# Kernel tuning notes

Hardware: AMD Instinct MI355X
Metric: run time of the kernel (lower is better)

Reference implementation:

```python
import jax, jax.numpy as jnp
import numpy as np
from jax import lax

WIN_SIZE = 11
WIN_SIGMA = 1.5
DATA_RANGE = 1.0
K1, K2 = 0.01, 0.03


def _gauss_1d(win_size, sigma):
    coords = jnp.arange(win_size, dtype=jnp.float32) - win_size // 2
    g = jnp.exp(-(coords ** 2) / (2.0 * sigma ** 2))
    return g / jnp.sum(g)


def _gauss_filter(x, win):
    # Separable depthwise gaussian blur, VALID padding (matches pytorch_msssim).
    C = x.shape[1]
    kh = jnp.tile(win.reshape(1, 1, -1, 1), (C, 1, 1, 1))  # (C,1,k,1)
    kw = jnp.tile(win.reshape(1, 1, 1, -1), (C, 1, 1, 1))  # (C,1,1,k)
    dn = ('NCHW', 'OIHW', 'NCHW')
    x = lax.conv_general_dilated(x, kh, (1, 1), 'VALID',
                                 dimension_numbers=dn, feature_group_count=C)
    x = lax.conv_general_dilated(x, kw, (1, 1), 'VALID',
                                 dimension_numbers=dn, feature_group_count=C)
    return x


def _ssim(X, Y, win, data_range):
    C1 = (K1 * data_range) ** 2
    C2 = (K2 * data_range) ** 2
    mu1 = _gauss_filter(X, win)
    mu2 = _gauss_filter(Y, win)
    mu1_sq = mu1 * mu1
    mu2_sq = mu2 * mu2
    mu1_mu2 = mu1 * mu2
    sigma1_sq = _gauss_filter(X * X, win) - mu1_sq
    sigma2_sq = _gauss_filter(Y * Y, win) - mu2_sq
    sigma12 = _gauss_filter(X * Y, win) - mu1_mu2
    cs_map = (2.0 * sigma12 + C2) / (sigma1_sq + sigma2_sq + C2)
    ssim_map = ((2.0 * mu1_mu2 + C1) / (mu1_sq + mu2_sq + C1)) * cs_map
    return jnp.mean(ssim_map)


def setup_inputs() -> dict:
    key = jax.random.key(0)
    k1, k2 = jax.random.split(key)
    shape = (16, 3, 384, 512)
    pred = jax.random.uniform(k1, shape, dtype=jnp.float32)
    target = jax.random.uniform(k2, shape, dtype=jnp.float32)
    return {"pred": pred, "target": target}


def reference(pred, target):
    win = _gauss_1d(WIN_SIZE, WIN_SIGMA)
    ssim_val = _ssim(pred, target, win, DATA_RANGE)
    return 1.0 - ssim_val
```

## Files before the change

### kernel.cpp

```cpp
#include <hip/hip_runtime.h>
#include <math.h>

#define WIN 11
#define IMG_H 384
#define IMG_W 512
#define OUT_H (IMG_H - WIN + 1)
#define OUT_W (IMG_W - WIN + 1)
#define RPW 2
#define NPAIRS 187
#define NIMG 48
#define TOTAL_PAIRS (NPAIRS * NIMG)
#define WPB 4
#define NBLOCKS 2248
#define BPX 281
#define NBUCKETS 256

typedef float v2 __attribute__((ext_vector_type(2)));

struct GaussW { float g[WIN]; };

__device__ __forceinline__ v2 shfl_v2(v2 v, int src) {
    v2 r; r.x = __shfl(v.x, src, 64); r.y = __shfl(v.y, src, 64); return r;
}

__device__ __forceinline__ void horiz11_v2(const v2 (&A)[8], v2 (&out)[8],
                                           int lane, const GaussW& gw)
{
    v2 V[18];
    #pragma unroll
    for (int j = 0; j < 8; ++j) V[j] = A[j];
    #pragma unroll
    for (int j = 0; j < 8; ++j) V[8 + j] = shfl_v2(A[j], lane + 1);
    V[16] = shfl_v2(A[0], lane + 2);
    V[17] = shfl_v2(A[1], lane + 2);
    #pragma unroll
    for (int j = 0; j < 8; ++j) {
        v2 o = 0.f;
        #pragma unroll
        for (int k = 0; k < WIN; ++k) {
            v2 g = gw.g[k];
            o = __builtin_elementwise_fma(g, V[j + k], o);
        }
        out[j] = o;
    }
}

__device__ __forceinline__ void horiz11_f(const float (&A)[8], float (&out)[8],
                                          int lane, const GaussW& gw)
{
    float V[18];
    #pragma unroll
    for (int j = 0; j < 8; ++j) V[j] = A[j];
    #pragma unroll
    for (int j = 0; j < 8; ++j) V[8 + j] = __shfl(A[j], lane + 1, 64);
    V[16] = __shfl(A[0], lane + 2, 64);
    V[17] = __shfl(A[1], lane + 2, 64);
    #pragma unroll
    for (int j = 0; j < 8; ++j) {
        float o = 0.f;
        #pragma unroll
        for (int k = 0; k < WIN; ++k) o = fmaf(gw.g[k], V[j + k], o);
        out[j] = o;
    }
}

__global__ __launch_bounds__(256) void ssim_fused_kernel(
    const float* __restrict__ X, const float* __restrict__ Y,
    double* __restrict__ accum, GaussW gw)
{
    const int wave = threadIdx.x >> 6;
    const int lane = threadIdx.x & 63;

    const int id = blockIdx.x;
    const int wb = (id & 7) * BPX + (id >> 3);
    const int P  = wb * WPB + wave;
    if (P >= TOTAL_PAIRS) return;

    const int img  = P / NPAIRS;
    const int pair = P % NPAIRS;
    const int r0   = pair * RPW;
    const int c0   = lane << 3;
    const float* __restrict__ Xb = X + ((size_t)img * IMG_H + r0) * IMG_W + c0;
    const float* __restrict__ Yb = Y + ((size_t)img * IMG_H + r0) * IMG_W + c0;

    v2 a01[RPW][8], a23[RPW][8];
    float a4[RPW][8];
    #pragma unroll
    for (int r = 0; r < RPW; ++r)
        #pragma unroll
        for (int j = 0; j < 8; ++j) { a01[r][j] = 0.f; a23[r][j] = 0.f; a4[r][j] = 0.f; }

    #pragma unroll
    for (int k = 0; k < RPW + WIN - 1; ++k) {
        const float* rx = Xb + (size_t)k * IMG_W;
        const float* ry = Yb + (size_t)k * IMG_W;
        float4 xa = *(const float4*)(rx);
        float4 xb = *(const float4*)(rx + 4);
        float4 ya = *(const float4*)(ry);
        float4 yb = *(const float4*)(ry + 4);
        v2 p[8] = {{xa.x, ya.x}, {xa.y, ya.y}, {xa.z, ya.z}, {xa.w, ya.w},
                   {xb.x, yb.x}, {xb.y, yb.y}, {xb.z, yb.z}, {xb.w, yb.w}};
        #pragma unroll
        for (int r = 0; r < RPW; ++r) {
            if (k - r >= 0 && k - r < WIN) {
                v2 g = gw.g[k - r];
                #pragma unroll
                for (int j = 0; j < 8; ++j) {
                    v2 q = p[j];
                    a01[r][j] = __builtin_elementwise_fma(g, q, a01[r][j]);
                    v2 t = g * q;
                    a23[r][j] = __builtin_elementwise_fma(t, q, a23[r][j]);
                    a4[r][j]  = fmaf(t.x, q.y, a4[r][j]);
                }
            }
        }
    }

    const float C1 = 1e-4f, C2 = 9e-4f;
    float sum = 0.f;
    #pragma unroll
    for (int r = 0; r < RPW; ++r) {
        v2 h01[8], h23[8];
        float h4[8];
        horiz11_v2(a01[r], h01, lane, gw);
        horiz11_v2(a23[r], h23, lane, gw);
        horiz11_f (a4[r],  h4,  lane, gw);
        #pragma unroll
        for (int j = 0; j < 8; ++j) {
            v2 mu = h01[j];
            v2 sq = mu * mu;
            float m12 = mu.x * mu.y;
            v2 sig = h23[j] - sq;
            float s12 = h4[j] - m12;
            float num = fmaf(2.f, m12, C1) * fmaf(2.f, s12, C2);
            float den = (sq.x + sq.y + C1) * (sig.x + sig.y + C2);
            float ssim = num * __builtin_amdgcn_rcpf(den);
            sum += (c0 + j < OUT_W) ? ssim : 0.f;
        }
    }

    #pragma unroll
    for (int off = 32; off; off >>= 1)
        sum += __shfl_down(sum, off, 64);
    if (lane == 0)
        atomicAdd(&accum[P & (NBUCKETS - 1)], (double)sum);
}

__global__ void ssim_finalize_kernel(const double* __restrict__ accum,
                                     float* __restrict__ out, double inv_count)
{
    const int lane = threadIdx.x;
    double s = 0.0;
    for (int i = lane; i < NBUCKETS; i += 64) s += accum[i];
    #pragma unroll
    for (int off = 32; off; off >>= 1)
        s += __shfl_down(s, off, 64);
    if (lane == 0) out[0] = (float)(1.0 - s * inv_count);
}

extern "C" void kernel_launch(void* const* d_in, const int* in_sizes, int n_in,
                              void* d_out, int out_size, void* d_ws, size_t ws_size,
                              hipStream_t stream) {
    const float* X = (const float*)d_in[0];
    const float* Y = (const float*)d_in[1];
    float* out = (float*)d_out;
    double* accum = (double*)d_ws;

    GaussW gw;
    {
        double g[WIN], ssum = 0.0;
        for (int i = 0; i < WIN; ++i) {
            double d = (double)i - WIN / 2;
            g[i] = exp(-(d * d) / (2.0 * 1.5 * 1.5));
            ssum += g[i];
        }
        for (int i = 0; i < WIN; ++i) gw.g[i] = (float)(g[i] / ssum);
    }

    hipMemsetAsync(accum, 0, NBUCKETS * sizeof(double), stream);

    ssim_fused_kernel<<<NBLOCKS, 64 * WPB, 0, stream>>>(X, Y, accum, gw);

    const double inv_count = 1.0 / ((double)NIMG * OUT_H * OUT_W);
    ssim_finalize_kernel<<<1, 64, 0, stream>>>(accum, out, inv_count);
}
```

Before: 127.1 us.

## Stage block's input rows into LDS via global_load_lds before vertical pass

Each block now owns 8 contiguous output rows of one image and cooperatively copies the 18 needed X and Y rows into LDS using direct global-to-LDS loads. The vertical filter then reads from LDS instead of global memory. This removes the redundant global/L2 re-reads of overlapping halo rows between waves. In exchange it uses about 72KB of dynamic LDS per block, which limits occupancy, and adds a full wait plus barrier before any compute.

Result: no change. 125.9 us (-1.0%).

```diff
diff --git a/kernel.cpp b/kernel.cpp
--- a/kernel.cpp
+++ b/kernel.cpp
@@ -9,15 +9,27 @@
 #define RPW 2
 #define NPAIRS 187
 #define NIMG 48
-#define TOTAL_PAIRS (NPAIRS * NIMG)
 #define WPB 4
-#define NBLOCKS 2248
-#define BPX 281
+#define ROWS_PB (RPW * WPB)
+#define PB_PER_IMG 47
+#define NBLOCKS (NIMG * PB_PER_IMG)
+#define BPX 282
+#define STAGE_ROWS (ROWS_PB + WIN - 1)
+#define ROW_BYTES (IMG_W * 4)
+#define SLOT_BYTES (2 * ROW_BYTES)
+#define LDS_BYTES (STAGE_ROWS * SLOT_BYTES)
 #define NBUCKETS 256
 
 typedef float v2 __attribute__((ext_vector_type(2)));
 
 struct GaussW { float g[WIN]; };
+
+__device__ __forceinline__ void gload16(const void* g, void* l) {
+    __builtin_amdgcn_global_load_lds(
+        (const __attribute__((address_space(1))) unsigned int*)g,
+        (__attribute__((address_space(3))) unsigned int*)l,
+        16, 0, 0);
+}
 
 __device__ __forceinline__ v2 shfl_v2(v2 v, int src) {
     v2 r; r.x = __shfl(v.x, src, 64); r.y = __shfl(v.y, src, 64); return r;
@@ -68,82 +80,100 @@
     const float* __restrict__ X, const float* __restrict__ Y,
     double* __restrict__ accum, GaussW gw)
 {
+    extern __shared__ char smem[];
     const int wave = threadIdx.x >> 6;
     const int lane = threadIdx.x & 63;
 
     const int id = blockIdx.x;
     const int wb = (id & 7) * BPX + (id >> 3);
-    const int P  = wb * WPB + wave;
-    if (P >= TOTAL_PAIRS) return;
-
-    const int img  = P / NPAIRS;
-    const int pair = P % NPAIRS;
-    const int r0   = pair * RPW;
-    const int c0   = lane << 3;
-    const float* __restrict__ Xb = X + ((size_t)img * IMG_H + r0) * IMG_W + c0;
-    const float* __restrict__ Yb = Y + ((size_t)img * IMG_H + r0) * IMG_W + c0;
-
-    v2 a01[RPW][8], a23[RPW][8];
-    float a4[RPW][8];
-    #pragma unroll
-    for (int r = 0; r < RPW; ++r)
-        #pragma unroll
-        for (int j = 0; j < 8; ++j) { a01[r][j] = 0.f; a23[r][j] = 0.f; a4[r][j] = 0.f; }
-
-    #pragma unroll
-    for (int k = 0; k < RPW + WIN - 1; ++k) {
-        const float* rx = Xb + (size_t)k * IMG_W;
-        const float* ry = Yb + (size_t)k * IMG_W;
-        float4 xa = *(const float4*)(rx);
-        float4 xb = *(const float4*)(rx + 4);
-        float4 ya = *(const float4*)(ry);
-        float4 yb = *(const float4*)(ry + 4);
-        v2 p[8] = {{xa.x, ya.x}, {xa.y, ya.y}, {xa.z, ya.z}, {xa.w, ya.w},
-                   {xb.x, yb.x}, {xb.y, yb.y}, {xb.z, yb.z}, {xb.w, yb.w}};
-        #pragma unroll
-        for (int r = 0; r < RPW; ++r) {
-            if (k - r >= 0 && k - r < WIN) {
-                v2 g = gw.g[k - r];
-                #pragma unroll
-                for (int j = 0; j < 8; ++j) {
-                    v2 q = p[j];
-                    a01[r][j] = __builtin_elementwise_fma(g, q, a01[r][j]);
-                    v2 t = g * q;
-                    a23[r][j] = __builtin_elementwise_fma(t, q, a23[r][j]);
-                    a4[r][j]  = fmaf(t.x, q.y, a4[r][j]);
+    const int img = wb / PB_PER_IMG;
+    const int pb  = wb - img * PB_PER_IMG;
+    const int r0  = pb * ROWS_PB;
+
+    {
+        const int t = wave >> 1, e = wave & 1;
+        const float* tb = t ? Y : X;
+        const char* src = (const char*)(tb + (size_t)img * IMG_H * IMG_W)
+                          + lane * 32 + e * 16;
+        char* dst = smem + t * ROW_BYTES + e * 1024;
+        #pragma unroll
+        for (int r = 0; r < STAGE_ROWS; ++r) {
+            int row = r0 + r;
+            row = row < IMG_H ? row : (IMG_H - 1);
+            gload16(src + (size_t)row * ROW_BYTES, dst + r * SLOT_BYTES);
+        }
+    }
+    asm volatile("s_waitcnt vmcnt(0)" ::: "memory");
+    __syncthreads();
+
+    const int pair = pb * WPB + wave;
+    if (pair < NPAIRS) {
+        const int c0 = lane << 3;
+        const char* lb = smem + (2 * wave) * SLOT_BYTES + lane * 16;
+
+        v2 a01[RPW][8], a23[RPW][8];
+        float a4[RPW][8];
+        #pragma unroll
+        for (int r = 0; r < RPW; ++r)
+            #pragma unroll
+            for (int j = 0; j < 8; ++j) { a01[r][j] = 0.f; a23[r][j] = 0.f; a4[r][j] = 0.f; }
+
+        #pragma unroll
+        for (int k = 0; k < RPW + WIN - 1; ++k) {
+            const char* lr = lb + k * SLOT_BYTES;
+            float4 xa = *(const float4*)(lr);
+            float4 xb = *(const float4*)(lr + 1024);
+            float4 ya = *(const float4*)(lr + ROW_BYTES);
+            float4 yb = *(const float4*)(lr + ROW_BYTES + 1024);
+            v2 p[8] = {{xa.x, ya.x}, {xa.y, ya.y}, {xa.z, ya.z}, {xa.w, ya.w},
+                       {xb.x, yb.x}, {xb.y, yb.y}, {xb.z, yb.z}, {xb.w, yb.w}};
+            #pragma unroll
+            for (int r = 0; r < RPW; ++r) {
+                if (k - r >= 0 && k - r < WIN) {
+                    v2 g = gw.g[k - r];
+                    #pragma unroll
+                    for (int j = 0; j < 8; ++j) {
+                        v2 q = p[j];
+                        a01[r][j] = __builtin_elementwise_fma(g, q, a01[r][j]);
+                        v2 t = g * q;
+                        a23[r][j] = __builtin_elementwise_fma(t, q, a23[r][j]);
+                        a4[r][j]  = fmaf(t.x, q.y, a4[r][j]);
+                    }
                 }
             }
         }
-    }
-
-    const float C1 = 1e-4f, C2 = 9e-4f;
-    float sum = 0.f;
-    #pragma unroll
-    for (int r = 0; r < RPW; ++r) {
-        v2 h01[8], h23[8];
-        float h4[8];
-        horiz11_v2(a01[r], h01, lane, gw);
-        horiz11_v2(a23[r], h23, lane, gw);
-        horiz11_f (a4[r],  h4,  lane, gw);
-        #pragma unroll
-        for (int j = 0; j < 8; ++j) {
-            v2 mu = h01[j];
-            v2 sq = mu * mu;
-            float m12 = mu.x * mu.y;
-            v2 sig = h23[j] - sq;
-            float s12 = h4[j] - m12;
-            float num = fmaf(2.f, m12, C1) * fmaf(2.f, s12, C2);
-            float den = (sq.x + sq.y + C1) * (sig.x + sig.y + C2);
-            float ssim = num * __builtin_amdgcn_rcpf(den);
-            sum += (c0 + j < OUT_W) ? ssim : 0.f;
-        }
-    }
-
-    #pragma unroll
-    for (int off = 32; off; off >>= 1)
-        sum += __shfl_down(sum, off, 64);
-    if (lane == 0)
-        atomicAdd(&accum[P & (NBUCKETS - 1)], (double)sum);
+
+        const float C1 = 1e-4f, C2 = 9e-4f;
+        float sum = 0.f;
+        #pragma unroll
+        for (int r = 0; r < RPW; ++r) {
+            v2 h01[8], h23[8];
+            float h4[8];
+            horiz11_v2(a01[r], h01, lane, gw);
+            horiz11_v2(a23[r], h23, lane, gw);
+            horiz11_f (a4[r],  h4,  lane, gw);
+            #pragma unroll
+            for (int j = 0; j < 8; ++j) {
+                v2 mu = h01[j];
+                v2 sq = mu * mu;
+                float m12 = mu.x * mu.y;
+                v2 sig = h23[j] - sq;
+                float s12 = h4[j] - m12;
+                float num = fmaf(2.f, m12, C1) * fmaf(2.f, s12, C2);
+                float den = (sq.x + sq.y + C1) * (sig.x + sig.y + C2);
+                float ssim = num * __builtin_amdgcn_rcpf(den);
+                sum += (c0 + j < OUT_W) ? ssim : 0.f;
+            }
+        }
+
+        #pragma unroll
+        for (int off = 32; off; off >>= 1)
+            sum += __shfl_down(sum, off, 64);
+        if (lane == 0) {
+            const int P = img * NPAIRS + pair;
+            atomicAdd(&accum[P & (NBUCKETS - 1)], (double)sum);
+        }
+    }
 }
 
 __global__ void ssim_finalize_kernel(const double* __restrict__ accum,
@@ -177,9 +207,17 @@
         for (int i = 0; i < WIN; ++i) gw.g[i] = (float)(g[i] / ssum);
     }
 
+    static bool s_attr_done = false;
+    if (!s_attr_done) {
+        (void)hipFuncSetAttribute((const void*)ssim_fused_kernel,
+                                  hipFuncAttributeMaxDynamicSharedMemorySize,
+                                  LDS_BYTES);
+        s_attr_done = true;
+    }
+
     hipMemsetAsync(accum, 0, NBUCKETS * sizeof(double), stream);
 
-    ssim_fused_kernel<<<NBLOCKS, 64 * WPB, 0, stream>>>(X, Y, accum, gw);
+    ssim_fused_kernel<<<NBLOCKS, 64 * WPB, LDS_BYTES, stream>>>(X, Y, accum, gw);
 
     const double inv_count = 1.0 / ((double)NIMG * OUT_H * OUT_W);
     ssim_finalize_kernel<<<1, 64, 0, stream>>>(accum, out, inv_count);
```
